# Optimization experiments

Measured on AMD Instinct MI355X. Metric: run time of the kernel, lower is better.

## Reference

```python
import jax, jax.numpy as jnp
import numpy as np

DIM = 1024
HEADS = 16
HEAD_DIM = DIM // HEADS


def setup_inputs() -> dict:
    key = jax.random.key(0)
    ks = jax.random.split(key, 5)
    s = 1.0 / np.sqrt(DIM)
    x = jax.random.normal(ks[0], (2, 2048, DIM), dtype=jnp.float32)
    # torch nn.Linear weights are [out_features, in_features]
    W_qkv = jax.random.uniform(ks[1], (3 * DIM, DIM), dtype=jnp.float32, minval=-s, maxval=s)
    b_qkv = jax.random.uniform(ks[2], (3 * DIM,), dtype=jnp.float32, minval=-s, maxval=s)
    W_out = jax.random.uniform(ks[3], (DIM, DIM), dtype=jnp.float32, minval=-s, maxval=s)
    b_out = jax.random.uniform(ks[4], (DIM,), dtype=jnp.float32, minval=-s, maxval=s)
    return {"x": x, "W_qkv": W_qkv, "b_qkv": b_qkv, "W_out": W_out, "b_out": b_out}


def reference(x, W_qkv, b_qkv, W_out, b_out):
    B, N, D = x.shape
    qkv = jnp.einsum('bnd,ed->bne', x, W_qkv) + b_qkv            # [B,N,3D]
    qkv = qkv.reshape(B, N, 3, HEADS, HEAD_DIM)
    qkv = jnp.transpose(qkv, (2, 0, 3, 1, 4))                    # [3,B,H,N,hd]
    q, k, v = qkv[0], qkv[1], qkv[2]
    scale = 1.0 / np.sqrt(HEAD_DIM).astype(np.float32)
    attn = jnp.einsum('bhnd,bhmd->bhnm', q, k) * scale           # [B,H,N,N]
    attn = jax.nn.softmax(attn, axis=-1)
    out = jnp.einsum('bhnm,bhmd->bhnd', attn, v)                 # [B,H,N,hd]
    out = jnp.transpose(out, (0, 2, 1, 3)).reshape(B, N, D)
    out = jnp.einsum('bnd,ed->bne', out, W_out) + b_out
    return out
```

## Files before the change

kernel.cpp:

```cpp
#include <hip/hip_runtime.h>
#include <stdint.h>
#include <stddef.h>

typedef __attribute__((ext_vector_type(4))) float  f32x4;
typedef __attribute__((ext_vector_type(8))) short  s16x8;
typedef __attribute__((ext_vector_type(4))) float  float4v;
typedef __attribute__((ext_vector_type(4))) unsigned short u16x4;

#define DIM    1024
#define HEADS  16
#define HD     64
#define SEQ    2048
#define BATCH  2
#define TOKENS (BATCH * SEQ)

#define QSCALE 0.18033688011112042f

__device__ __forceinline__ unsigned short f2bf(float f) {
  union { float f; uint32_t u; } x; x.f = f;
  uint32_t r = x.u + 0x7fffu + ((x.u >> 16) & 1u);
  return (unsigned short)(r >> 16);
}

__device__ __forceinline__ float fast_exp2(float x) {
#if __has_builtin(__builtin_amdgcn_exp2f)
  return __builtin_amdgcn_exp2f(x);
#else
  return exp2f(x);
#endif
}

__device__ __forceinline__ void stage16(const unsigned short* gp, unsigned short* lp) {
#if __has_builtin(__builtin_amdgcn_global_load_lds)
  __builtin_amdgcn_global_load_lds((const __attribute__((address_space(1))) void*)gp,
                                   (__attribute__((address_space(3))) void*)lp, 16, 0, 0);
#else
  *(s16x8*)(lp + (threadIdx.x & 63) * 8) = *(const s16x8*)gp;
#endif
}

#define N4_X  (TOKENS * DIM / 4)
#define N4_WQ (3 * DIM * DIM / 4)
#define N4_WO (DIM * DIM / 4)
__global__ __launch_bounds__(256) void mhsa_cast_all(const float* __restrict__ x,
    const float* __restrict__ wq, const float* __restrict__ wo,
    unsigned short* __restrict__ xb, unsigned short* __restrict__ wqb,
    unsigned short* __restrict__ wob) {
  int i = blockIdx.x * 256 + threadIdx.x;
  const float* src; unsigned short* dst; int off;
  if (i < N4_X)              { src = x;  dst = xb;  off = i; }
  else if (i < N4_X + N4_WQ) { src = wq; dst = wqb; off = i - N4_X; }
  else                       { src = wo; dst = wob; off = i - (N4_X + N4_WQ); }
  float4v f = ((const float4v*)src)[off];
  u16x4 o;
  o.x = f2bf(f.x); o.y = f2bf(f.y); o.z = f2bf(f.z); o.w = f2bf(f.w);
  ((u16x4*)dst)[off] = o;
}

__global__ __launch_bounds__(256) void mhsa_gemm_qkv(const unsigned short* __restrict__ A,
    const unsigned short* __restrict__ Bw, const float* __restrict__ bias,
    unsigned short* __restrict__ qws, unsigned short* __restrict__ kws,
    unsigned short* __restrict__ vws) {
  __shared__ unsigned short As[128 * 32];
  __shared__ unsigned short Bs[128 * 32];
  const int t = threadIdx.x;
  const int w = t >> 6, l = t & 63;
  const int wm = w >> 1, wn = w & 1;
  const int rowBase = blockIdx.y * 128;
  const int colBase = blockIdx.x * 128;
  const int fr = l & 15, fc = (l >> 4) * 8;
  const int crow = l >> 2, ccol = (l & 3) * 8;

  f32x4 zero = {0.f, 0.f, 0.f, 0.f};
  f32x4 acc[4][4];
  #pragma unroll
  for (int i = 0; i < 4; ++i)
    #pragma unroll
    for (int j = 0; j < 4; ++j) acc[i][j] = zero;

  for (int k0 = 0; k0 < DIM; k0 += 32) {
    __syncthreads();
    #pragma unroll
    for (int it = 0; it < 2; ++it) {
      const int c = w * 2 + it;
      stage16(A  + (size_t)(rowBase + c * 16 + crow) * DIM + k0 + ccol, &As[c * 512]);
      stage16(Bw + (size_t)(colBase + c * 16 + crow) * DIM + k0 + ccol, &Bs[c * 512]);
    }
    __syncthreads();
    s16x8 af[4], bfr[4];
    #pragma unroll
    for (int i = 0; i < 4; ++i) af[i]  = *(const s16x8*)&As[(wm * 64 + i * 16 + fr) * 32 + fc];
    #pragma unroll
    for (int j = 0; j < 4; ++j) bfr[j] = *(const s16x8*)&Bs[(wn * 64 + j * 16 + fr) * 32 + fc];
    #pragma unroll
    for (int i = 0; i < 4; ++i)
      #pragma unroll
      for (int j = 0; j < 4; ++j)
        acc[i][j] = __builtin_amdgcn_mfma_f32_16x16x32_bf16(af[i], bfr[j], acc[i][j], 0, 0, 0);
  }

  const int q4 = l >> 4, ln = l & 15;
  #pragma unroll
  for (int i = 0; i < 4; ++i) {
    const int trow0 = rowBase + wm * 64 + i * 16 + q4 * 4;
    #pragma unroll
    for (int j = 0; j < 4; ++j) {
      const int e = colBase + wn * 64 + j * 16 + ln;
      const float bs = bias[e];
      const int which = e >> 10;
      const int rr = e & 1023;
      const int h = rr >> 6, d = rr & 63;
      unsigned short* dst = (which == 0) ? qws : ((which == 1) ? kws : vws);
      const float sc = (which == 0) ? QSCALE : 1.0f;
      #pragma unroll
      for (int r = 0; r < 4; ++r) {
        const int trow = trow0 + r;
        const int b = trow >> 11, n = trow & 2047;
        const float val = (acc[i][j][r] + bs) * sc;
        size_t idx;
        if (which == 2) idx = ((size_t)((b * HEADS + h) * HD + d)) * SEQ + n;
        else            idx = ((size_t)((b * HEADS + h) * SEQ + n)) * HD + d;
        dst[idx] = f2bf(val);
      }
    }
  }
}

__global__ __launch_bounds__(256) void mhsa_gemm_out(const unsigned short* __restrict__ A,
    const unsigned short* __restrict__ Bw, const float* __restrict__ bias,
    float* __restrict__ out) {
  __shared__ unsigned short As[128 * 32];
  __shared__ unsigned short Bs[128 * 32];
  const int t = threadIdx.x;
  const int w = t >> 6, l = t & 63;
  const int wm = w >> 1, wn = w & 1;
  const int rowBase = blockIdx.y * 128;
  const int colBase = blockIdx.x * 128;
  const int fr = l & 15, fc = (l >> 4) * 8;
  const int crow = l >> 2, ccol = (l & 3) * 8;

  f32x4 zero = {0.f, 0.f, 0.f, 0.f};
  f32x4 acc[4][4];
  #pragma unroll
  for (int i = 0; i < 4; ++i)
    #pragma unroll
    for (int j = 0; j < 4; ++j) acc[i][j] = zero;

  for (int k0 = 0; k0 < DIM; k0 += 32) {
    __syncthreads();
    #pragma unroll
    for (int it = 0; it < 2; ++it) {
      const int c = w * 2 + it;
      stage16(A  + (size_t)(rowBase + c * 16 + crow) * DIM + k0 + ccol, &As[c * 512]);
      stage16(Bw + (size_t)(colBase + c * 16 + crow) * DIM + k0 + ccol, &Bs[c * 512]);
    }
    __syncthreads();
    s16x8 af[4], bfr[4];
    #pragma unroll
    for (int i = 0; i < 4; ++i) af[i]  = *(const s16x8*)&As[(wm * 64 + i * 16 + fr) * 32 + fc];
    #pragma unroll
    for (int j = 0; j < 4; ++j) bfr[j] = *(const s16x8*)&Bs[(wn * 64 + j * 16 + fr) * 32 + fc];
    #pragma unroll
    for (int i = 0; i < 4; ++i)
      #pragma unroll
      for (int j = 0; j < 4; ++j)
        acc[i][j] = __builtin_amdgcn_mfma_f32_16x16x32_bf16(af[i], bfr[j], acc[i][j], 0, 0, 0);
  }

  const int q4 = l >> 4, ln = l & 15;
  #pragma unroll
  for (int i = 0; i < 4; ++i) {
    const int trow0 = rowBase + wm * 64 + i * 16 + q4 * 4;
    #pragma unroll
    for (int j = 0; j < 4; ++j) {
      const int e = colBase + wn * 64 + j * 16 + ln;
      const float bs = bias[e];
      #pragma unroll
      for (int r = 0; r < 4; ++r)
        out[(size_t)(trow0 + r) * DIM + e] = acc[i][j][r] + bs;
    }
  }
}

__global__ __launch_bounds__(256, 2) void mhsa_attn(const unsigned short* __restrict__ q,
    const unsigned short* __restrict__ k, const unsigned short* __restrict__ vt,
    unsigned short* __restrict__ o) {
  __shared__ unsigned short Qs[128 * 64];
  __shared__ unsigned short Ps[4 * 32 * 68];
  __shared__ unsigned short Ks[2][64 * 64];
  __shared__ unsigned short Vs[2][64 * 64];
  const int t = threadIdx.x, w = t >> 6, l = t & 63;
  const int q4 = l >> 4, ln = l & 15;
  const int bh = blockIdx.y, q0 = blockIdx.x * 128;
  const unsigned short* qb  = q  + (size_t)bh * SEQ * HD;
  const unsigned short* kb  = k  + (size_t)bh * SEQ * HD;
  const unsigned short* vtb = vt + (size_t)bh * HD * SEQ;

  const int srow = l >> 3;
  const int scol = ((l & 7) ^ srow) * 8;

  #pragma unroll
  for (int it = 0; it < 4; ++it) {
    const int c = w * 4 + it;
    stage16(qb + (size_t)(q0 + c * 8 + srow) * HD + scol, &Qs[c * 512]);
  }
  #pragma unroll
  for (int it = 0; it < 2; ++it) {
    const int c = w + it * 4;
    stage16(kb  + (size_t)(c * 8 + srow) * HD + scol, &Ks[0][c * 512]);
    stage16(vtb + (size_t)(c * 8 + srow) * SEQ + scol, &Vs[0][c * 512]);
  }
  __syncthreads();

  s16x8 aq[2][2];
  #pragma unroll
  for (int i = 0; i < 2; ++i)
    #pragma unroll
    for (int kk = 0; kk < 2; ++kk)
      aq[i][kk] = *(const s16x8*)&Qs[(w * 32 + i * 16 + ln) * 64 + (((kk * 4 + q4) ^ (ln & 7)) * 8)];

  unsigned short* Pw = &Ps[w * (32 * 68)];
  f32x4 zero = {0.f, 0.f, 0.f, 0.f};
  f32x4 accO[2][4];
  float lsum[2][4];
  #pragma unroll
  for (int i = 0; i < 2; ++i)
    #pragma unroll
    for (int jd = 0; jd < 4; ++jd) { accO[i][jd] = zero; lsum[i][jd] = 0.f; }

  for (int jt = 0; jt < SEQ / 64; ++jt) {
    const int cur = jt & 1, nxt = cur ^ 1;
    if (jt + 1 < SEQ / 64) {
      const int j1 = (jt + 1) * 64;
      #pragma unroll
      for (int it = 0; it < 2; ++it) {
        const int c = w + it * 4;
        stage16(kb  + (size_t)(j1 + c * 8 + srow) * HD + scol, &Ks[nxt][c * 512]);
        stage16(vtb + (size_t)(c * 8 + srow) * SEQ + j1 + scol, &Vs[nxt][c * 512]);
      }
    }

    f32x4 S[2][4];
    #pragma unroll
    for (int i = 0; i < 2; ++i)
      #pragma unroll
      for (int j = 0; j < 4; ++j) S[i][j] = zero;
    #pragma unroll
    for (int j = 0; j < 4; ++j) {
      s16x8 bk0 = *(const s16x8*)&Ks[cur][(j * 16 + ln) * 64 + ((q4 ^ (ln & 7)) * 8)];
      s16x8 bk1 = *(const s16x8*)&Ks[cur][(j * 16 + ln) * 64 + (((4 + q4) ^ (ln & 7)) * 8)];
      #pragma unroll
      for (int i = 0; i < 2; ++i) {
        S[i][j] = __builtin_amdgcn_mfma_f32_16x16x32_bf16(aq[i][0], bk0, S[i][j], 0, 0, 0);
        S[i][j] = __builtin_amdgcn_mfma_f32_16x16x32_bf16(aq[i][1], bk1, S[i][j], 0, 0, 0);
      }
    }

    #pragma unroll
    for (int i = 0; i < 2; ++i)
      #pragma unroll
      for (int j = 0; j < 4; ++j)
        #pragma unroll
        for (int r = 0; r < 4; ++r) {
          float p = fast_exp2(S[i][j][r]);
          uint32_t u = __float_as_uint(p);
          lsum[i][r] += __uint_as_float(u & 0xffff0000u);
          Pw[(i * 16 + q4 * 4 + r) * 68 + j * 16 + ln] = (unsigned short)(u >> 16);
        }

    s16x8 ap[2][2];
    #pragma unroll
    for (int i = 0; i < 2; ++i)
      #pragma unroll
      for (int kk = 0; kk < 2; ++kk)
        ap[i][kk] = *(const s16x8*)&Pw[(i * 16 + ln) * 68 + kk * 32 + q4 * 8];

    #pragma unroll
    for (int jd = 0; jd < 4; ++jd) {
      s16x8 bv0 = *(const s16x8*)&Vs[cur][(jd * 16 + ln) * 64 + ((q4 ^ (ln & 7)) * 8)];
      s16x8 bv1 = *(const s16x8*)&Vs[cur][(jd * 16 + ln) * 64 + (((4 + q4) ^ (ln & 7)) * 8)];
      #pragma unroll
      for (int i = 0; i < 2; ++i) {
        accO[i][jd] = __builtin_amdgcn_mfma_f32_16x16x32_bf16(ap[i][0], bv0, accO[i][jd], 0, 0, 0);
        accO[i][jd] = __builtin_amdgcn_mfma_f32_16x16x32_bf16(ap[i][1], bv1, accO[i][jd], 0, 0, 0);
      }
    }

    __syncthreads();
  }

  const int b = bh >> 4, h = bh & 15;
  #pragma unroll
  for (int i = 0; i < 2; ++i)
    #pragma unroll
    for (int r = 0; r < 4; ++r) {
      float s = lsum[i][r];
      #pragma unroll
      for (int m = 1; m < 16; m <<= 1) s += __shfl_xor(s, m);
      const float inv = 1.f / s;
      const int row = q0 + w * 32 + i * 16 + q4 * 4 + r;
      #pragma unroll
      for (int jd = 0; jd < 4; ++jd)
        o[((size_t)(b * SEQ + row)) * DIM + h * HD + jd * 16 + ln] = f2bf(accO[i][jd][r] * inv);
    }
}

extern "C" void kernel_launch(void* const* d_in, const int* in_sizes, int n_in,
                              void* d_out, int out_size, void* d_ws, size_t ws_size,
                              hipStream_t stream) {
  const float* x     = (const float*)d_in[0];
  const float* Wqkv  = (const float*)d_in[1];
  const float* bqkv  = (const float*)d_in[2];
  const float* Wout  = (const float*)d_in[3];
  const float* bout  = (const float*)d_in[4];
  float* out = (float*)d_out;

  unsigned short* ws = (unsigned short*)d_ws;
  unsigned short* x_bf    = ws;
  unsigned short* wqkv_bf = x_bf    + (size_t)TOKENS * DIM;
  unsigned short* wout_bf = wqkv_bf + (size_t)3 * DIM * DIM;
  unsigned short* q_ws    = wout_bf + (size_t)DIM * DIM;
  unsigned short* k_ws    = q_ws    + (size_t)TOKENS * DIM;
  unsigned short* v_ws    = k_ws    + (size_t)TOKENS * DIM;
  unsigned short* ao_ws   = v_ws    + (size_t)TOKENS * DIM;

  {
    const int n4 = N4_X + N4_WQ + N4_WO;
    mhsa_cast_all<<<n4 / 256, 256, 0, stream>>>(x, Wqkv, Wout, x_bf, wqkv_bf, wout_bf);
  }

  {
    dim3 grid(3 * DIM / 128, TOKENS / 128);
    mhsa_gemm_qkv<<<grid, 256, 0, stream>>>(x_bf, wqkv_bf, bqkv, q_ws, k_ws, v_ws);
  }

  {
    dim3 grid(SEQ / 128, BATCH * HEADS);
    mhsa_attn<<<grid, 256, 0, stream>>>(q_ws, k_ws, v_ws, ao_ws);
  }

  {
    dim3 grid(DIM / 128, TOKENS / 128);
    mhsa_gemm_out<<<grid, 256, 0, stream>>>(ao_ws, wout_bf, bout, out);
  }
}
```

Baseline: 223.5 us.

## Transpose MFMA operand order for vectorized epilogues and packed P stores

Both GEMMs swap the MFMA operands so each lane holds four consecutive output features for one token. This lets the bias load, the Q/K bf16 stores and the fp32 output stores become 4-wide vector accesses instead of scalar stores. In attention, S is computed transposed so each lane packs four bf16 probabilities with a perm and writes them as a single 8-byte LDS store. The row sum then needs only two cross-lane shuffles, and Q staging shares the P buffer to cut shared memory. The V-transpose store stays scalar, and the new P write pattern with a 72-element stride may change LDS bank conflicts.

```diff
diff --git a/kernel.cpp b/kernel.cpp
--- a/kernel.cpp
+++ b/kernel.cpp
@@ -6,6 +6,7 @@
 typedef __attribute__((ext_vector_type(8))) short  s16x8;
 typedef __attribute__((ext_vector_type(4))) float  float4v;
 typedef __attribute__((ext_vector_type(4))) unsigned short u16x4;
+typedef __attribute__((ext_vector_type(2))) unsigned int   u32x2;
 
 #define DIM    1024
 #define HEADS  16
@@ -27,6 +28,14 @@
   return __builtin_amdgcn_exp2f(x);
 #else
   return exp2f(x);
+#endif
+}
+
+__device__ __forceinline__ uint32_t pack_bf16_trunc(uint32_t lo, uint32_t hi) {
+#if __has_builtin(__builtin_amdgcn_perm)
+  return __builtin_amdgcn_perm(hi, lo, 0x07060302u);
+#else
+  return (hi & 0xffff0000u) | (lo >> 16);
 #endif
 }
 
@@ -74,9 +83,9 @@
   f32x4 zero = {0.f, 0.f, 0.f, 0.f};
   f32x4 acc[4][4];
   #pragma unroll
-  for (int i = 0; i < 4; ++i)
-    #pragma unroll
-    for (int j = 0; j < 4; ++j) acc[i][j] = zero;
+  for (int a = 0; a < 4; ++a)
+    #pragma unroll
+    for (int b = 0; b < 4; ++b) acc[a][b] = zero;
 
   for (int k0 = 0; k0 < DIM; k0 += 32) {
     __syncthreads();
@@ -87,40 +96,43 @@
       stage16(Bw + (size_t)(colBase + c * 16 + crow) * DIM + k0 + ccol, &Bs[c * 512]);
     }
     __syncthreads();
-    s16x8 af[4], bfr[4];
-    #pragma unroll
-    for (int i = 0; i < 4; ++i) af[i]  = *(const s16x8*)&As[(wm * 64 + i * 16 + fr) * 32 + fc];
-    #pragma unroll
-    for (int j = 0; j < 4; ++j) bfr[j] = *(const s16x8*)&Bs[(wn * 64 + j * 16 + fr) * 32 + fc];
-    #pragma unroll
-    for (int i = 0; i < 4; ++i)
-      #pragma unroll
-      for (int j = 0; j < 4; ++j)
-        acc[i][j] = __builtin_amdgcn_mfma_f32_16x16x32_bf16(af[i], bfr[j], acc[i][j], 0, 0, 0);
+    s16x8 xf[4], wf[4];
+    #pragma unroll
+    for (int b = 0; b < 4; ++b) xf[b] = *(const s16x8*)&As[(wm * 64 + b * 16 + fr) * 32 + fc];
+    #pragma unroll
+    for (int a = 0; a < 4; ++a) wf[a] = *(const s16x8*)&Bs[(wn * 64 + a * 16 + fr) * 32 + fc];
+    #pragma unroll
+    for (int a = 0; a < 4; ++a)
+      #pragma unroll
+      for (int b = 0; b < 4; ++b)
+        acc[a][b] = __builtin_amdgcn_mfma_f32_16x16x32_bf16(wf[a], xf[b], acc[a][b], 0, 0, 0);
   }
 
   const int q4 = l >> 4, ln = l & 15;
-  #pragma unroll
-  for (int i = 0; i < 4; ++i) {
-    const int trow0 = rowBase + wm * 64 + i * 16 + q4 * 4;
-    #pragma unroll
-    for (int j = 0; j < 4; ++j) {
-      const int e = colBase + wn * 64 + j * 16 + ln;
-      const float bs = bias[e];
-      const int which = e >> 10;
-      const int rr = e & 1023;
-      const int h = rr >> 6, d = rr & 63;
-      unsigned short* dst = (which == 0) ? qws : ((which == 1) ? kws : vws);
-      const float sc = (which == 0) ? QSCALE : 1.0f;
-      #pragma unroll
-      for (int r = 0; r < 4; ++r) {
-        const int trow = trow0 + r;
-        const int b = trow >> 11, n = trow & 2047;
-        const float val = (acc[i][j][r] + bs) * sc;
-        size_t idx;
-        if (which == 2) idx = ((size_t)((b * HEADS + h) * HD + d)) * SEQ + n;
-        else            idx = ((size_t)((b * HEADS + h) * SEQ + n)) * HD + d;
-        dst[idx] = f2bf(val);
+  const int which = colBase >> 10;
+  const float sc = (which == 0) ? QSCALE : 1.0f;
+  unsigned short* dst = (which == 0) ? qws : ((which == 1) ? kws : vws);
+
+  #pragma unroll
+  for (int a = 0; a < 4; ++a) {
+    const int e0 = colBase + wn * 64 + a * 16 + q4 * 4;
+    const float4v bs4 = *(const float4v*)&bias[e0];
+    const int rr0 = e0 & 1023;
+    const int h = rr0 >> 6, d0 = rr0 & 63;
+    #pragma unroll
+    for (int b = 0; b < 4; ++b) {
+      const int tok = rowBase + wm * 64 + b * 16 + ln;
+      const int bb = tok >> 11, n = tok & 2047;
+      if (which != 2) {
+        u16x4 pk;
+        #pragma unroll
+        for (int r = 0; r < 4; ++r) pk[r] = f2bf((acc[a][b][r] + bs4[r]) * sc);
+        *(u16x4*)&dst[(((size_t)(bb * HEADS + h)) * SEQ + n) * HD + d0] = pk;
+      } else {
+        #pragma unroll
+        for (int r = 0; r < 4; ++r)
+          dst[(((size_t)(bb * HEADS + h)) * HD + d0 + r) * SEQ + n] =
+              f2bf(acc[a][b][r] + bs4[r]);
       }
     }
   }
@@ -142,9 +154,9 @@
   f32x4 zero = {0.f, 0.f, 0.f, 0.f};
   f32x4 acc[4][4];
   #pragma unroll
-  for (int i = 0; i < 4; ++i)
-    #pragma unroll
-    for (int j = 0; j < 4; ++j) acc[i][j] = zero;
+  for (int a = 0; a < 4; ++a)
+    #pragma unroll
+    for (int b = 0; b < 4; ++b) acc[a][b] = zero;
 
   for (int k0 = 0; k0 < DIM; k0 += 32) {
     __syncthreads();
@@ -155,29 +167,30 @@
       stage16(Bw + (size_t)(colBase + c * 16 + crow) * DIM + k0 + ccol, &Bs[c * 512]);
     }
     __syncthreads();
-    s16x8 af[4], bfr[4];
-    #pragma unroll
-    for (int i = 0; i < 4; ++i) af[i]  = *(const s16x8*)&As[(wm * 64 + i * 16 + fr) * 32 + fc];
-    #pragma unroll
-    for (int j = 0; j < 4; ++j) bfr[j] = *(const s16x8*)&Bs[(wn * 64 + j * 16 + fr) * 32 + fc];
-    #pragma unroll
-    for (int i = 0; i < 4; ++i)
-      #pragma unroll
-      for (int j = 0; j < 4; ++j)
-        acc[i][j] = __builtin_amdgcn_mfma_f32_16x16x32_bf16(af[i], bfr[j], acc[i][j], 0, 0, 0);
+    s16x8 xf[4], wf[4];
+    #pragma unroll
+    for (int b = 0; b < 4; ++b) xf[b] = *(const s16x8*)&As[(wm * 64 + b * 16 + fr) * 32 + fc];
+    #pragma unroll
+    for (int a = 0; a < 4; ++a) wf[a] = *(const s16x8*)&Bs[(wn * 64 + a * 16 + fr) * 32 + fc];
+    #pragma unroll
+    for (int a = 0; a < 4; ++a)
+      #pragma unroll
+      for (int b = 0; b < 4; ++b)
+        acc[a][b] = __builtin_amdgcn_mfma_f32_16x16x32_bf16(wf[a], xf[b], acc[a][b], 0, 0, 0);
   }
 
   const int q4 = l >> 4, ln = l & 15;
   #pragma unroll
-  for (int i = 0; i < 4; ++i) {
-    const int trow0 = rowBase + wm * 64 + i * 16 + q4 * 4;
-    #pragma unroll
-    for (int j = 0; j < 4; ++j) {
-      const int e = colBase + wn * 64 + j * 16 + ln;
-      const float bs = bias[e];
-      #pragma unroll
-      for (int r = 0; r < 4; ++r)
-        out[(size_t)(trow0 + r) * DIM + e] = acc[i][j][r] + bs;
+  for (int a = 0; a < 4; ++a) {
+    const int e0 = colBase + wn * 64 + a * 16 + q4 * 4;
+    const float4v bs4 = *(const float4v*)&bias[e0];
+    #pragma unroll
+    for (int b = 0; b < 4; ++b) {
+      const int tok = rowBase + wm * 64 + b * 16 + ln;
+      float4v v;
+      #pragma unroll
+      for (int r = 0; r < 4; ++r) v[r] = acc[a][b][r] + bs4[r];
+      *(float4v*)&out[(size_t)tok * DIM + e0] = v;
     }
   }
 }
@@ -185,8 +198,7 @@
 __global__ __launch_bounds__(256, 2) void mhsa_attn(const unsigned short* __restrict__ q,
     const unsigned short* __restrict__ k, const unsigned short* __restrict__ vt,
     unsigned short* __restrict__ o) {
-  __shared__ unsigned short Qs[128 * 64];
-  __shared__ unsigned short Ps[4 * 32 * 68];
+  __shared__ unsigned short QPs[4 * 32 * 72];
   __shared__ unsigned short Ks[2][64 * 64];
   __shared__ unsigned short Vs[2][64 * 64];
   const int t = threadIdx.x, w = t >> 6, l = t & 63;
@@ -199,11 +211,11 @@
   const int srow = l >> 3;
   const int scol = ((l & 7) ^ srow) * 8;
 
-  #pragma unroll
-  for (int it = 0; it < 4; ++it) {
-    const int c = w * 4 + it;
-    stage16(qb + (size_t)(q0 + c * 8 + srow) * HD + scol, &Qs[c * 512]);
-  }
+  unsigned short* Pw = &QPs[w * (32 * 72)];
+
+  #pragma unroll
+  for (int it = 0; it < 4; ++it)
+    stage16(qb + (size_t)(q0 + w * 32 + it * 8 + srow) * HD + scol, &Pw[it * 512]);
   #pragma unroll
   for (int it = 0; it < 2; ++it) {
     const int c = w + it * 4;
@@ -217,16 +229,15 @@
   for (int i = 0; i < 2; ++i)
     #pragma unroll
     for (int kk = 0; kk < 2; ++kk)
-      aq[i][kk] = *(const s16x8*)&Qs[(w * 32 + i * 16 + ln) * 64 + (((kk * 4 + q4) ^ (ln & 7)) * 8)];
-
-  unsigned short* Pw = &Ps[w * (32 * 68)];
+      aq[i][kk] = *(const s16x8*)&Pw[(i * 16 + ln) * 64 + (((kk * 4 + q4) ^ (ln & 7)) * 8)];
+
   f32x4 zero = {0.f, 0.f, 0.f, 0.f};
   f32x4 accO[2][4];
-  float lsum[2][4];
+  float lsum[2] = {0.f, 0.f};
   #pragma unroll
   for (int i = 0; i < 2; ++i)
     #pragma unroll
-    for (int jd = 0; jd < 4; ++jd) { accO[i][jd] = zero; lsum[i][jd] = 0.f; }
+    for (int jd = 0; jd < 4; ++jd) accO[i][jd] = zero;
 
   for (int jt = 0; jt < SEQ / 64; ++jt) {
     const int cur = jt & 1, nxt = cur ^ 1;
@@ -240,40 +251,44 @@
       }
     }
 
-    f32x4 S[2][4];
+    f32x4 St[4][2];
+    #pragma unroll
+    for (int jb = 0; jb < 4; ++jb)
+      #pragma unroll
+      for (int i = 0; i < 2; ++i) St[jb][i] = zero;
+    #pragma unroll
+    for (int jb = 0; jb < 4; ++jb) {
+      s16x8 ak0 = *(const s16x8*)&Ks[cur][(jb * 16 + ln) * 64 + ((q4 ^ (ln & 7)) * 8)];
+      s16x8 ak1 = *(const s16x8*)&Ks[cur][(jb * 16 + ln) * 64 + (((4 + q4) ^ (ln & 7)) * 8)];
+      #pragma unroll
+      for (int i = 0; i < 2; ++i) {
+        St[jb][i] = __builtin_amdgcn_mfma_f32_16x16x32_bf16(ak0, aq[i][0], St[jb][i], 0, 0, 0);
+        St[jb][i] = __builtin_amdgcn_mfma_f32_16x16x32_bf16(ak1, aq[i][1], St[jb][i], 0, 0, 0);
+      }
+    }
+
     #pragma unroll
     for (int i = 0; i < 2; ++i)
       #pragma unroll
-      for (int j = 0; j < 4; ++j) S[i][j] = zero;
-    #pragma unroll
-    for (int j = 0; j < 4; ++j) {
-      s16x8 bk0 = *(const s16x8*)&Ks[cur][(j * 16 + ln) * 64 + ((q4 ^ (ln & 7)) * 8)];
-      s16x8 bk1 = *(const s16x8*)&Ks[cur][(j * 16 + ln) * 64 + (((4 + q4) ^ (ln & 7)) * 8)];
-      #pragma unroll
-      for (int i = 0; i < 2; ++i) {
-        S[i][j] = __builtin_amdgcn_mfma_f32_16x16x32_bf16(aq[i][0], bk0, S[i][j], 0, 0, 0);
-        S[i][j] = __builtin_amdgcn_mfma_f32_16x16x32_bf16(aq[i][1], bk1, S[i][j], 0, 0, 0);
-      }
-    }
-
+      for (int jb = 0; jb < 4; ++jb) {
+        uint32_t u0 = __float_as_uint(fast_exp2(St[jb][i][0]));
+        uint32_t u1 = __float_as_uint(fast_exp2(St[jb][i][1]));
+        uint32_t u2 = __float_as_uint(fast_exp2(St[jb][i][2]));
+        uint32_t u3 = __float_as_uint(fast_exp2(St[jb][i][3]));
+        lsum[i] += __uint_as_float(u0 & 0xffff0000u) + __uint_as_float(u1 & 0xffff0000u)
+                 + __uint_as_float(u2 & 0xffff0000u) + __uint_as_float(u3 & 0xffff0000u);
+        u32x2 pk;
+        pk.x = pack_bf16_trunc(u0, u1);
+        pk.y = pack_bf16_trunc(u2, u3);
+        *(u32x2*)&Pw[(i * 16 + ln) * 72 + jb * 16 + q4 * 4] = pk;
+      }
+
+    s16x8 ap[2][2];
     #pragma unroll
     for (int i = 0; i < 2; ++i)
       #pragma unroll
-      for (int j = 0; j < 4; ++j)
-        #pragma unroll
-        for (int r = 0; r < 4; ++r) {
-          float p = fast_exp2(S[i][j][r]);
-          uint32_t u = __float_as_uint(p);
-          lsum[i][r] += __uint_as_float(u & 0xffff0000u);
-          Pw[(i * 16 + q4 * 4 + r) * 68 + j * 16 + ln] = (unsigned short)(u >> 16);
-        }
-
-    s16x8 ap[2][2];
-    #pragma unroll
-    for (int i = 0; i < 2; ++i)
-      #pragma unroll
       for (int kk = 0; kk < 2; ++kk)
-        ap[i][kk] = *(const s16x8*)&Pw[(i * 16 + ln) * 68 + kk * 32 + q4 * 8];
+        ap[i][kk] = *(const s16x8*)&Pw[(i * 16 + ln) * 72 + kk * 32 + q4 * 8];
 
     #pragma unroll
     for (int jd = 0; jd < 4; ++jd) {
@@ -291,18 +306,20 @@
 
   const int b = bh >> 4, h = bh & 15;
   #pragma unroll
-  for (int i = 0; i < 2; ++i)
+  for (int i = 0; i < 2; ++i) {
+    float s = lsum[i];
+    s += __shfl_xor(s, 16);
+    s += __shfl_xor(s, 32);
+    const float inv = 1.f / s;
     #pragma unroll
     for (int r = 0; r < 4; ++r) {
-      float s = lsum[i][r];
-      #pragma unroll
-      for (int m = 1; m < 16; m <<= 1) s += __shfl_xor(s, m);
-      const float inv = 1.f / s;
+      const float invr = __shfl(inv, (l & 48) + q4 * 4 + r);
       const int row = q0 + w * 32 + i * 16 + q4 * 4 + r;
       #pragma unroll
       for (int jd = 0; jd < 4; ++jd)
-        o[((size_t)(b * SEQ + row)) * DIM + h * HD + jd * 16 + ln] = f2bf(accO[i][jd][r] * inv);
-    }
+        o[((size_t)(b * SEQ + row)) * DIM + h * HD + jd * 16 + ln] = f2bf(accO[i][jd][r] * invr);
+    }
+  }
 }
 
 extern "C" void kernel_launch(void* const* d_in, const int* in_sizes, int n_in,
```

Measured after the change: 212.1 us. 5.1% less time.
